# Performance work log

Hardware: AMD Instinct MI355X
Metric: run time of the kernel (lower is better)

## Reference

```python
import jax, jax.numpy as jnp
import numpy as np

B, N, IN_F, OUT_F, H = 4, 1024, 256, 256, 8
HID = OUT_F // H  # 32
ALPHA = 0.2  # leaky relu negative slope


def setup_inputs() -> dict:
    key = jax.random.key(0)
    k1, k2, k3, k4 = jax.random.split(key, 4)
    h = jax.random.normal(k1, (B, N, IN_F), dtype=jnp.float32)
    # linear: in_features -> n_heads*n_hidden, no bias (stored as [in, out])
    W = jax.random.normal(k2, (IN_F, H * HID), dtype=jnp.float32) / np.sqrt(IN_F)
    # attn: Linear(2*n_hidden, 1, bias=False), shared across heads
    attn_w = jax.random.normal(k3, (2 * HID,), dtype=jnp.float32) / np.sqrt(2 * HID)
    # random dense adjacency (p=0.5) plus self loops, broadcast over heads
    u = jax.random.uniform(k4, (B, N, N, 1), dtype=jnp.float32)
    adj_mat = jnp.maximum((u < 0.5).astype(jnp.float32), jnp.eye(N, dtype=jnp.float32)[None, :, :, None])
    return {"h": h, "adj_mat": adj_mat, "W": W, "attn_w": attn_w}


def reference(h, adj_mat, W, attn_w):
    # g: [b, n, h, d]
    g = (h @ W).reshape(B, N, H, HID)
    # attn(concat(g_i, g_j)) decomposes: e[b,i,j,h] = <attn_w[:HID], g_i> + <attn_w[HID:], g_j>
    # (exactly the math of the repeat/repeat_interleave/cat + 1-wide linear, without the N^2 concat)
    e_i = jnp.einsum('bnhd,d->bnh', g, attn_w[:HID])   # g_repeat_interleave part (index i)
    e_j = jnp.einsum('bnhd,d->bnh', g, attn_w[HID:])   # g_repeat part (index j)
    e = e_i[:, :, None, :] + e_j[:, None, :, :]        # [b, i, j, h]
    e = jnp.where(e >= 0, e, ALPHA * e)                # LeakyReLU(alpha)
    e = jnp.where(adj_mat == 0, -jnp.inf, e)           # masked_fill
    a = jax.nn.softmax(e, axis=1)                      # faithful: original uses Softmax(dim=1)
    # dropout p acts as identity in eval mode / p=0
    out = jnp.einsum('bijh,bjhd->bihd', a, g)          # [b, i, h, d]
    return out.reshape(B, N, H * HID)                  # is_concat=True
```

## Files before the change

kernel.cpp:

```cpp
#include <hip/hip_runtime.h>
#include <math.h>

#define BB 4
#define NN 1024
#define HH 8
#define NROW (BB*NN)

typedef short s8v __attribute__((ext_vector_type(8)));
typedef float f4v __attribute__((ext_vector_type(4)));

__device__ __forceinline__ short bf16rne(float f) {
    unsigned u = __float_as_uint(f);
    u += 0x7FFF + ((u >> 16) & 1u);
    return (short)(u >> 16);
}

__global__ __launch_bounds__(256) void k_gemm_ei(const float* __restrict__ hm,
                                                 const float* __restrict__ W,
                                                 const float* __restrict__ aw,
                                                 float* __restrict__ g,
                                                 float* __restrict__ EFi,
                                                 float* __restrict__ EFj,
                                                 float* __restrict__ EFjt) {
    __shared__ __align__(16) float hs[8][256];
    __shared__ float aws[64];
    const int row0 = blockIdx.x * 8;
    const int t = threadIdx.x;
    if (t < 64) aws[t] = aw[t];
    const float4* h4 = (const float4*)(hm + row0 * 256);
    float4* hs4 = (float4*)&hs[0][0];
    hs4[t] = h4[t];
    hs4[t + 256] = h4[t + 256];
    __syncthreads();

    float acc[8];
#pragma unroll
    for (int r = 0; r < 8; ++r) acc[r] = 0.f;
    for (int k4 = 0; k4 < 64; ++k4) {
        const float w0 = W[(4 * k4 + 0) * 256 + t];
        const float w1 = W[(4 * k4 + 1) * 256 + t];
        const float w2 = W[(4 * k4 + 2) * 256 + t];
        const float w3 = W[(4 * k4 + 3) * 256 + t];
#pragma unroll
        for (int r = 0; r < 8; ++r) {
            const float4 hv = *(const float4*)&hs[r][4 * k4];
            acc[r] = fmaf(hv.x, w0, acc[r]);
            acc[r] = fmaf(hv.y, w1, acc[r]);
            acc[r] = fmaf(hv.z, w2, acc[r]);
            acc[r] = fmaf(hv.w, w3, acc[r]);
        }
    }
    const int d = t & 31, hh = t >> 5;
    const int b = row0 >> 10;
#pragma unroll
    for (int r = 0; r < 8; ++r) {
        g[(row0 + r) * 256 + t] = acc[r];
        float vi = acc[r] * aws[d];
        float vj = acc[r] * aws[32 + d];
#pragma unroll
        for (int mm = 1; mm < 32; mm <<= 1) {
            vi += __shfl_xor(vi, mm);
            vj += __shfl_xor(vj, mm);
        }
        if (d == 0) {
            const int row = row0 + r;
            const float Ei = __expf(vi), Fi = __expf(0.2f * vi);
            const float Ej = __expf(vj), Fj = __expf(0.2f * vj);
            *(float2*)&EFi[(size_t)row * 16 + hh * 2] = make_float2(Ei, Fi);
            *(float2*)&EFj[(size_t)row * 16 + hh * 2] = make_float2(Ej, Fj);
            const int n = row & (NN - 1);
            EFjt[((size_t)(b * 8 + hh) * 2 + 0) * NN + n] = Ej;
            EFjt[((size_t)(b * 8 + hh) * 2 + 1) * NN + n] = Fj;
        }
    }
}

__global__ __launch_bounds__(256) void k_s(const float* __restrict__ adj,
                                           const float* __restrict__ EFi,
                                           const float* __restrict__ EFj,
                                           float* __restrict__ ps) {
    __shared__ __align__(16) float eis[128 * 16];
    __shared__ float sp[4][8][64];
    const int bx = blockIdx.x;
    const int b = bx >> 7, jc = (bx >> 3) & 15, ic = bx & 7;
    const int j0 = jc * 64, i0 = ic * 128;
    const int t = threadIdx.x;

    const float4* src4 = (const float4*)(EFi + (size_t)(b * NN + i0) * 16);
    ((float4*)eis)[t] = src4[t];
    ((float4*)eis)[t + 256] = src4[t + 256];

    const int ii = t >> 6, jj = t & 63;
    const float* ej = EFj + (size_t)(b * NN + j0 + jj) * 16;
    const float4 f0 = *(const float4*)&ej[0];
    const float4 f1 = *(const float4*)&ej[4];
    const float4 f2 = *(const float4*)&ej[8];
    const float4 f3 = *(const float4*)&ej[12];
    const float ejE0 = f0.x, ejF0 = f0.y, ejE1 = f0.z, ejF1 = f0.w;
    const float ejE2 = f1.x, ejF2 = f1.y, ejE3 = f1.z, ejF3 = f1.w;
    const float ejE4 = f2.x, ejF4 = f2.y, ejE5 = f2.z, ejF5 = f2.w;
    const float ejE6 = f3.x, ejF6 = f3.y, ejE7 = f3.z, ejF7 = f3.w;
    __syncthreads();

    float s0 = 0.f, s1 = 0.f, s2 = 0.f, s3 = 0.f;
    float s4 = 0.f, s5 = 0.f, s6 = 0.f, s7 = 0.f;
    const float* adjp = adj + (size_t)b * NN * NN + j0 + jj;
    for (int i = ii; i < 128; i += 4) {
        const float a = adjp[(size_t)(i0 + i) * NN];
        const float4 x0 = *(const float4*)&eis[i * 16];
        const float4 x1 = *(const float4*)&eis[i * 16 + 4];
        const float4 x2 = *(const float4*)&eis[i * 16 + 8];
        const float4 x3 = *(const float4*)&eis[i * 16 + 12];
        s0 = fmaf(a, fmaxf(x0.x * ejE0, x0.y * ejF0), s0);
        s1 = fmaf(a, fmaxf(x0.z * ejE1, x0.w * ejF1), s1);
        s2 = fmaf(a, fmaxf(x1.x * ejE2, x1.y * ejF2), s2);
        s3 = fmaf(a, fmaxf(x1.z * ejE3, x1.w * ejF3), s3);
        s4 = fmaf(a, fmaxf(x2.x * ejE4, x2.y * ejF4), s4);
        s5 = fmaf(a, fmaxf(x2.z * ejE5, x2.w * ejF5), s5);
        s6 = fmaf(a, fmaxf(x3.x * ejE6, x3.y * ejF6), s6);
        s7 = fmaf(a, fmaxf(x3.z * ejE7, x3.w * ejF7), s7);
    }
    sp[ii][0][jj] = s0; sp[ii][1][jj] = s1; sp[ii][2][jj] = s2; sp[ii][3][jj] = s3;
    sp[ii][4][jj] = s4; sp[ii][5][jj] = s5; sp[ii][6][jj] = s6; sp[ii][7][jj] = s7;
    __syncthreads();
#pragma unroll
    for (int k = 0; k < 2; ++k) {
        const int idx = t * 2 + k;
        const int jjo = idx >> 3, h = idx & 7;
        const float s = sp[0][h][jjo] + sp[1][h][jjo] + sp[2][h][jjo] + sp[3][h][jjo];
        ps[ic * (NROW * 8) + (b * NN + j0 + jjo) * 8 + h] = s;
    }
}

__global__ __launch_bounds__(256) void k_prep(const float* __restrict__ ps,
                                              const float* __restrict__ g,
                                              short* __restrict__ Gt) {
    __shared__ float rss[16][8];
    const int bx = blockIdx.x;
    const int b = bx >> 6, j0 = (bx & 63) * 16;
    const int t = threadIdx.x;
    if (t < 128) {
        const int jj = t >> 3, h = t & 7;
        float s = 0.f;
#pragma unroll
        for (int ic = 0; ic < 8; ++ic)
            s += ps[ic * (NROW * 8) + (b * NN + j0 + jj) * 8 + h];
        rss[jj][h] = 1.0f / s;
    }
    __syncthreads();
    const int h = t >> 5, d = t & 31;
    unsigned short v16[16];
#pragma unroll
    for (int r = 0; r < 16; ++r) {
        const float val = g[(size_t)(b * NN + j0 + r) * 256 + t] * rss[r][h];
        v16[r] = (unsigned short)bf16rne(val);
    }
    const int jt = j0 >> 5, jj0 = j0 & 31;
    short* dst = Gt + ((size_t)((b * 8 + h) * 32 + jt)) * 1024 + d * 32 + jj0;
    uint4 w0, w1;
    w0.x = (unsigned)v16[0] | ((unsigned)v16[1] << 16);
    w0.y = (unsigned)v16[2] | ((unsigned)v16[3] << 16);
    w0.z = (unsigned)v16[4] | ((unsigned)v16[5] << 16);
    w0.w = (unsigned)v16[6] | ((unsigned)v16[7] << 16);
    w1.x = (unsigned)v16[8] | ((unsigned)v16[9] << 16);
    w1.y = (unsigned)v16[10] | ((unsigned)v16[11] << 16);
    w1.z = (unsigned)v16[12] | ((unsigned)v16[13] << 16);
    w1.w = (unsigned)v16[14] | ((unsigned)v16[15] << 16);
    *(uint4*)dst = w0;
    *(uint4*)(dst + 8) = w1;
}

__global__ __launch_bounds__(256) void k_out_mfma(const float* __restrict__ adj,
                                                  const short* __restrict__ Gt,
                                                  const float* __restrict__ EFi,
                                                  const float* __restrict__ EFjt,
                                                  float* __restrict__ out) {
    __shared__ short gts[4][4][32][40];
    __shared__ float ejt[4][2][128];
    const int bx = blockIdx.x;
    const int hs = bx >> 8, b = (bx >> 6) & 3, i0 = (bx & 63) * 16;
    const int t = threadIdx.x;
    const int wave = t >> 6, lane = t & 63;
    const int m = lane & 15, q = lane >> 4;
    const int h = hs * 4 + wave;

    const float2 eif = *(const float2*)&EFi[(size_t)(b * NN + i0 + m) * 16 + h * 2];
    const float EiV = eif.x, FiV = eif.y;
    f4v acc0 = {0.f, 0.f, 0.f, 0.f}, acc1 = {0.f, 0.f, 0.f, 0.f};

    const float* adjrow = adj + (size_t)b * NN * NN + (size_t)(i0 + m) * NN;
    const float4* gtg4 = (const float4*)Gt;
    const float4* ejt4 = (const float4*)(EFjt + (size_t)b * 8 * 2 * NN);

    for (int s = 0; s < 8; ++s) {
        float4 g0, g1, g2, g3, g4, g5, g6, g7;
#define LG(k)                                                                     \
        {                                                                         \
            const int u = t + 256 * (k);                                          \
            g##k = gtg4[(size_t)(b * 8 + hs * 4 + (u >> 9)) * 4096 + s * 512 +    \
                        (u & 511)];                                               \
        }
        LG(0) LG(1) LG(2) LG(3) LG(4) LG(5) LG(6) LG(7)
#undef LG
        f4v a0, a1, a2, a3, a4, a5, a6, a7;
#define LA(k2, lt, half)                                                          \
        a##k2 = *(const f4v*)&adjrow[s * 128 + (lt) * 32 + q * 8 + (half) * 4];
        LA(0, 0, 0) LA(1, 0, 1) LA(2, 1, 0) LA(3, 1, 1)
        LA(4, 2, 0) LA(5, 2, 1) LA(6, 3, 0) LA(7, 3, 1)
#undef LA
        const float4 ev =
            ejt4[(size_t)((hs * 4 + (t >> 6)) * 2 + ((t >> 5) & 1)) * 256 +
                 s * 32 + (t & 31)];
        __syncthreads();
#define SG(k)                                                                     \
        {                                                                         \
            const int u = t + 256 * (k);                                          \
            char* dstp = (char*)gts + (u >> 9) * 10240 + ((u >> 7) & 3) * 2560 +  \
                         ((u >> 2) & 31) * 80 + (u & 3) * 16;                     \
            *(float4*)dstp = g##k;                                                \
        }
        SG(0) SG(1) SG(2) SG(3) SG(4) SG(5) SG(6) SG(7)
#undef SG
        *(float4*)&ejt[t >> 6][(t >> 5) & 1][(t & 31) * 4] = ev;
        __syncthreads();

#define LT(lt, aA, aB)                                                            \
        {                                                                         \
            const f4v ejA = *(const f4v*)&ejt[wave][0][(lt) * 32 + q * 8];        \
            const f4v ejB = *(const f4v*)&ejt[wave][0][(lt) * 32 + q * 8 + 4];    \
            const f4v fjA = *(const f4v*)&ejt[wave][1][(lt) * 32 + q * 8];        \
            const f4v fjB = *(const f4v*)&ejt[wave][1][(lt) * 32 + q * 8 + 4];    \
            const float p0 = aA[0] * fmaxf(EiV * ejA[0], FiV * fjA[0]);           \
            const float p1 = aA[1] * fmaxf(EiV * ejA[1], FiV * fjA[1]);           \
            const float p2 = aA[2] * fmaxf(EiV * ejA[2], FiV * fjA[2]);           \
            const float p3 = aA[3] * fmaxf(EiV * ejA[3], FiV * fjA[3]);           \
            const float p4 = aB[0] * fmaxf(EiV * ejB[0], FiV * fjB[0]);           \
            const float p5 = aB[1] * fmaxf(EiV * ejB[1], FiV * fjB[1]);           \
            const float p6 = aB[2] * fmaxf(EiV * ejB[2], FiV * fjB[2]);           \
            const float p7 = aB[3] * fmaxf(EiV * ejB[3], FiV * fjB[3]);           \
            unsigned w0, w1, w2, w3;                                              \
            asm("v_cvt_pk_bf16_f32 %0, %1, %2" : "=v"(w0) : "v"(p0), "v"(p1));    \
            asm("v_cvt_pk_bf16_f32 %0, %1, %2" : "=v"(w1) : "v"(p2), "v"(p3));    \
            asm("v_cvt_pk_bf16_f32 %0, %1, %2" : "=v"(w2) : "v"(p4), "v"(p5));    \
            asm("v_cvt_pk_bf16_f32 %0, %1, %2" : "=v"(w3) : "v"(p6), "v"(p7));    \
            union { unsigned u[4]; s8v v; } Au;                                   \
            Au.u[0] = w0; Au.u[1] = w1; Au.u[2] = w2; Au.u[3] = w3;               \
            const s8v A = Au.v;                                                   \
            const s8v B0 = *(const s8v*)&gts[wave][lt][m][q * 8];                 \
            const s8v B1 = *(const s8v*)&gts[wave][lt][m + 16][q * 8];            \
            acc0 = __builtin_amdgcn_mfma_f32_16x16x32_bf16(A, B0, acc0, 0, 0, 0); \
            acc1 = __builtin_amdgcn_mfma_f32_16x16x32_bf16(A, B1, acc1, 0, 0, 0); \
        }
        LT(0, a0, a1) LT(1, a2, a3) LT(2, a4, a5) LT(3, a6, a7)
#undef LT
    }

    float* op = out + (size_t)(b * NN + i0) * 256;
#pragma unroll
    for (int r = 0; r < 4; ++r) {
        const int row = q * 4 + r;
        op[(size_t)row * 256 + h * 32 + m] = acc0[r];
        op[(size_t)row * 256 + h * 32 + 16 + m] = acc1[r];
    }
}

extern "C" void kernel_launch(void* const* d_in, const int* in_sizes, int n_in,
                              void* d_out, int out_size, void* d_ws, size_t ws_size,
                              hipStream_t stream) {
    const float* h      = (const float*)d_in[0];
    const float* adj    = (const float*)d_in[1];
    const float* W      = (const float*)d_in[2];
    const float* attn_w = (const float*)d_in[3];
    float* out = (float*)d_out;

    float* ws = (float*)d_ws;
    float* g    = ws;
    float* EFi  = g + NROW * 256;
    float* EFj  = EFi + NROW * 16;
    float* EFjt = EFj + NROW * 16;
    float* ps   = EFjt + NROW * 16;
    short* Gt   = (short*)(ps + 8 * NROW * 8);

    k_gemm_ei<<<NROW / 8, 256, 0, stream>>>(h, W, attn_w, g, EFi, EFj, EFjt);
    k_s<<<512, 256, 0, stream>>>(adj, EFi, EFj, ps);
    k_prep<<<256, 256, 0, stream>>>(ps, g, Gt);
    k_out_mfma<<<512, 256, 0, stream>>>(adj, Gt, EFi, EFjt, out);
}
```

Baseline: 124.4 us.

## Drop prep kernel: write bf16 G directly, atomically reduce softmax denominators

The GEMM kernel now writes unnormalized g straight into the bf16 transposed Gt layout and zeroes a denominator buffer, removing the fp32 g buffer and the separate prep kernel. The column-sum kernel accumulates its partial sums with atomic adds into a single Dt array instead of per-chunk partials. The output kernel divides the per-j exp factors by the denominator as it loads them, so normalization moves from G onto the attention weights. This removes one launch and the fp32 g round trip, at the cost of atomics, per-element divides in the hot loop, and a bf16 rounding of unnormalized g.

```diff
diff --git a/kernel.cpp b/kernel.cpp
--- a/kernel.cpp
+++ b/kernel.cpp
@@ -14,19 +14,26 @@
     u += 0x7FFF + ((u >> 16) & 1u);
     return (short)(u >> 16);
 }
+__device__ __forceinline__ unsigned pk2(float a, float b) {
+    return ((unsigned)(unsigned short)bf16rne(a)) |
+           (((unsigned)(unsigned short)bf16rne(b)) << 16);
+}
 
 __global__ __launch_bounds__(256) void k_gemm_ei(const float* __restrict__ hm,
                                                  const float* __restrict__ W,
                                                  const float* __restrict__ aw,
-                                                 float* __restrict__ g,
+                                                 short* __restrict__ Gt,
                                                  float* __restrict__ EFi,
-                                                 float* __restrict__ EFj,
-                                                 float* __restrict__ EFjt) {
+                                                 float* __restrict__ EFjt,
+                                                 float* __restrict__ Dt) {
     __shared__ __align__(16) float hs[8][256];
     __shared__ float aws[64];
     const int row0 = blockIdx.x * 8;
     const int t = threadIdx.x;
-    if (t < 64) aws[t] = aw[t];
+    if (t < 64) {
+        aws[t] = aw[t];
+        Dt[blockIdx.x * 64 + t] = 0.f;
+    }
     const float4* h4 = (const float4*)(hm + row0 * 256);
     float4* hs4 = (float4*)&hs[0][0];
     hs4[t] = h4[t];
@@ -52,9 +59,21 @@
     }
     const int d = t & 31, hh = t >> 5;
     const int b = row0 >> 10;
+
+    {
+        const int n0 = row0 & (NN - 1);
+        short* dst = Gt + ((size_t)((b * 8 + hh) * 32 + (n0 >> 5))) * 1024 +
+                     d * 32 + (n0 & 31);
+        uint4 w;
+        w.x = pk2(acc[0], acc[1]);
+        w.y = pk2(acc[2], acc[3]);
+        w.z = pk2(acc[4], acc[5]);
+        w.w = pk2(acc[6], acc[7]);
+        *(uint4*)dst = w;
+    }
+
 #pragma unroll
     for (int r = 0; r < 8; ++r) {
-        g[(row0 + r) * 256 + t] = acc[r];
         float vi = acc[r] * aws[d];
         float vj = acc[r] * aws[32 + d];
 #pragma unroll
@@ -64,21 +83,19 @@
         }
         if (d == 0) {
             const int row = row0 + r;
-            const float Ei = __expf(vi), Fi = __expf(0.2f * vi);
-            const float Ej = __expf(vj), Fj = __expf(0.2f * vj);
-            *(float2*)&EFi[(size_t)row * 16 + hh * 2] = make_float2(Ei, Fi);
-            *(float2*)&EFj[(size_t)row * 16 + hh * 2] = make_float2(Ej, Fj);
             const int n = row & (NN - 1);
-            EFjt[((size_t)(b * 8 + hh) * 2 + 0) * NN + n] = Ej;
-            EFjt[((size_t)(b * 8 + hh) * 2 + 1) * NN + n] = Fj;
-        }
-    }
-}
-
-__global__ __launch_bounds__(256) void k_s(const float* __restrict__ adj,
-                                           const float* __restrict__ EFi,
-                                           const float* __restrict__ EFj,
-                                           float* __restrict__ ps) {
+            *(float2*)&EFi[(size_t)row * 16 + hh * 2] =
+                make_float2(__expf(vi), __expf(0.2f * vi));
+            EFjt[((size_t)(b * 8 + hh) * 2 + 0) * NN + n] = __expf(vj);
+            EFjt[((size_t)(b * 8 + hh) * 2 + 1) * NN + n] = __expf(0.2f * vj);
+        }
+    }
+}
+
+__global__ __launch_bounds__(256) void k_den(const float* __restrict__ adj,
+                                             const float* __restrict__ EFi,
+                                             const float* __restrict__ EFjt,
+                                             float* __restrict__ Dt) {
     __shared__ __align__(16) float eis[128 * 16];
     __shared__ float sp[4][8][64];
     const int bx = blockIdx.x;
@@ -91,15 +108,15 @@
     ((float4*)eis)[t + 256] = src4[t + 256];
 
     const int ii = t >> 6, jj = t & 63;
-    const float* ej = EFj + (size_t)(b * NN + j0 + jj) * 16;
-    const float4 f0 = *(const float4*)&ej[0];
-    const float4 f1 = *(const float4*)&ej[4];
-    const float4 f2 = *(const float4*)&ej[8];
-    const float4 f3 = *(const float4*)&ej[12];
-    const float ejE0 = f0.x, ejF0 = f0.y, ejE1 = f0.z, ejF1 = f0.w;
-    const float ejE2 = f1.x, ejF2 = f1.y, ejE3 = f1.z, ejF3 = f1.w;
-    const float ejE4 = f2.x, ejF4 = f2.y, ejE5 = f2.z, ejF5 = f2.w;
-    const float ejE6 = f3.x, ejF6 = f3.y, ejE7 = f3.z, ejF7 = f3.w;
+    const float* ejb = EFjt + (size_t)b * 16 * NN + j0 + jj;
+    const float ejE0 = ejb[0 * NN],  ejF0 = ejb[1 * NN];
+    const float ejE1 = ejb[2 * NN],  ejF1 = ejb[3 * NN];
+    const float ejE2 = ejb[4 * NN],  ejF2 = ejb[5 * NN];
+    const float ejE3 = ejb[6 * NN],  ejF3 = ejb[7 * NN];
+    const float ejE4 = ejb[8 * NN],  ejF4 = ejb[9 * NN];
+    const float ejE5 = ejb[10 * NN], ejF5 = ejb[11 * NN];
+    const float ejE6 = ejb[12 * NN], ejF6 = ejb[13 * NN];
+    const float ejE7 = ejb[14 * NN], ejF7 = ejb[15 * NN];
     __syncthreads();
 
     float s0 = 0.f, s1 = 0.f, s2 = 0.f, s3 = 0.f;
@@ -126,54 +143,18 @@
 #pragma unroll
     for (int k = 0; k < 2; ++k) {
         const int idx = t * 2 + k;
-        const int jjo = idx >> 3, h = idx & 7;
-        const float s = sp[0][h][jjo] + sp[1][h][jjo] + sp[2][h][jjo] + sp[3][h][jjo];
-        ps[ic * (NROW * 8) + (b * NN + j0 + jjo) * 8 + h] = s;
-    }
-}
-
-__global__ __launch_bounds__(256) void k_prep(const float* __restrict__ ps,
-                                              const float* __restrict__ g,
-                                              short* __restrict__ Gt) {
-    __shared__ float rss[16][8];
-    const int bx = blockIdx.x;
-    const int b = bx >> 6, j0 = (bx & 63) * 16;
-    const int t = threadIdx.x;
-    if (t < 128) {
-        const int jj = t >> 3, h = t & 7;
-        float s = 0.f;
-#pragma unroll
-        for (int ic = 0; ic < 8; ++ic)
-            s += ps[ic * (NROW * 8) + (b * NN + j0 + jj) * 8 + h];
-        rss[jj][h] = 1.0f / s;
-    }
-    __syncthreads();
-    const int h = t >> 5, d = t & 31;
-    unsigned short v16[16];
-#pragma unroll
-    for (int r = 0; r < 16; ++r) {
-        const float val = g[(size_t)(b * NN + j0 + r) * 256 + t] * rss[r][h];
-        v16[r] = (unsigned short)bf16rne(val);
-    }
-    const int jt = j0 >> 5, jj0 = j0 & 31;
-    short* dst = Gt + ((size_t)((b * 8 + h) * 32 + jt)) * 1024 + d * 32 + jj0;
-    uint4 w0, w1;
-    w0.x = (unsigned)v16[0] | ((unsigned)v16[1] << 16);
-    w0.y = (unsigned)v16[2] | ((unsigned)v16[3] << 16);
-    w0.z = (unsigned)v16[4] | ((unsigned)v16[5] << 16);
-    w0.w = (unsigned)v16[6] | ((unsigned)v16[7] << 16);
-    w1.x = (unsigned)v16[8] | ((unsigned)v16[9] << 16);
-    w1.y = (unsigned)v16[10] | ((unsigned)v16[11] << 16);
-    w1.z = (unsigned)v16[12] | ((unsigned)v16[13] << 16);
-    w1.w = (unsigned)v16[14] | ((unsigned)v16[15] << 16);
-    *(uint4*)dst = w0;
-    *(uint4*)(dst + 8) = w1;
+        const int jjo = idx >> 3, hq = idx & 7;
+        const float sv =
+            sp[0][hq][jjo] + sp[1][hq][jjo] + sp[2][hq][jjo] + sp[3][hq][jjo];
+        unsafeAtomicAdd(&Dt[(size_t)(b * 8 + hq) * NN + j0 + jjo], sv);
+    }
 }
 
 __global__ __launch_bounds__(256) void k_out_mfma(const float* __restrict__ adj,
                                                   const short* __restrict__ Gt,
                                                   const float* __restrict__ EFi,
                                                   const float* __restrict__ EFjt,
+                                                  const float* __restrict__ Dt,
                                                   float* __restrict__ out) {
     __shared__ short gts[4][4][32][40];
     __shared__ float ejt[4][2][128];
@@ -191,6 +172,7 @@
     const float* adjrow = adj + (size_t)b * NN * NN + (size_t)(i0 + m) * NN;
     const float4* gtg4 = (const float4*)Gt;
     const float4* ejt4 = (const float4*)(EFjt + (size_t)b * 8 * 2 * NN);
+    const float4* dt4  = (const float4*)(Dt + (size_t)b * 8 * NN);
 
     for (int s = 0; s < 8; ++s) {
         float4 g0, g1, g2, g3, g4, g5, g6, g7;
@@ -208,9 +190,11 @@
         LA(0, 0, 0) LA(1, 0, 1) LA(2, 1, 0) LA(3, 1, 1)
         LA(4, 2, 0) LA(5, 2, 1) LA(6, 3, 0) LA(7, 3, 1)
 #undef LA
-        const float4 ev =
+        float4 ev =
             ejt4[(size_t)((hs * 4 + (t >> 6)) * 2 + ((t >> 5) & 1)) * 256 +
                  s * 32 + (t & 31)];
+        const float4 dv = dt4[(size_t)(hs * 4 + (t >> 6)) * 256 + s * 32 + (t & 31)];
+        ev.x /= dv.x; ev.y /= dv.y; ev.z /= dv.z; ev.w /= dv.w;
         __syncthreads();
 #define SG(k)                                                                     \
         {                                                                         \
@@ -274,15 +258,12 @@
     float* out = (float*)d_out;
 
     float* ws = (float*)d_ws;
-    float* g    = ws;
-    float* EFi  = g + NROW * 256;
-    float* EFj  = EFi + NROW * 16;
-    float* EFjt = EFj + NROW * 16;
-    float* ps   = EFjt + NROW * 16;
-    short* Gt   = (short*)(ps + 8 * NROW * 8);
-
-    k_gemm_ei<<<NROW / 8, 256, 0, stream>>>(h, W, attn_w, g, EFi, EFj, EFjt);
-    k_s<<<512, 256, 0, stream>>>(adj, EFi, EFj, ps);
-    k_prep<<<256, 256, 0, stream>>>(ps, g, Gt);
-    k_out_mfma<<<512, 256, 0, stream>>>(adj, Gt, EFi, EFjt, out);
-}
+    short* Gt   = (short*)ws;
+    float* EFi  = ws + 1048576;
+    float* EFjt = EFi + NROW * 16;
+    float* Dt   = EFjt + NROW * 16;
+
+    k_gemm_ei<<<NROW / 8, 256, 0, stream>>>(h, W, attn_w, Gt, EFi, EFjt, Dt);
+    k_den<<<512, 256, 0, stream>>>(adj, EFi, EFjt, Dt);
+    k_out_mfma<<<512, 256, 0, stream>>>(adj, Gt, EFi, EFjt, Dt, out);
+}
```

New measurement: 122.2 us. No clear change (-1.8%).
